# Kernel optimization log

Hardware: AMD Instinct MI355X
Metric: run time of the kernel (lower is better)

The kernel has to match this reference:

```python
import jax, jax.numpy as jnp
import numpy as np

LOG2 = float(np.log(2.0))
CUTOFF = 10.0
N, E, H, F, G = 50000, 800000, 64, 64, 50


def ssp(x):
    # ShiftedSoftplus
    return jax.nn.softplus(x) - LOG2


def setup_inputs() -> dict:
    key = jax.random.key(0)
    ks = jax.random.split(key, 20)
    s = 0.05
    inp = {
        'x0': jax.random.normal(ks[0], (N, H), jnp.float32),
        'x1': jax.random.normal(ks[1], (N, H), jnp.float32),
        'edge_index0': jax.random.randint(ks[2], (2, E), 0, N, jnp.int32),
        'edge_index1': jax.random.randint(ks[3], (2, E), 0, N, jnp.int32),
        'edge_weight0': jax.random.uniform(ks[4], (E,), jnp.float32) * CUTOFF,
        'edge_weight1': jax.random.uniform(ks[5], (E,), jnp.float32) * CUTOFF,
        'edge_attr0': jax.random.uniform(ks[6], (E, G), jnp.float32),
        'edge_attr1': jax.random.uniform(ks[7], (E, G), jnp.float32),
        # shared filter MLP (num_gaussians -> num_filters -> num_filters)
        'mlp_w1': jax.random.normal(ks[8], (G, F), jnp.float32) * s,
        'mlp_b1': jnp.zeros((F,), jnp.float32),
        'mlp_w2': jax.random.normal(ks[9], (F, F), jnp.float32) * s,
        'mlp_b2': jnp.zeros((F,), jnp.float32),
        # per-edge-type CFConv lin1 (H->F, no bias) and lin2 (F->H, bias)
        'lin1_w0': jax.random.normal(ks[10], (H, F), jnp.float32) * s,
        'lin2_w0': jax.random.normal(ks[11], (F, H), jnp.float32) * s,
        'lin2_b0': jnp.zeros((H,), jnp.float32),
        'lin1_w1': jax.random.normal(ks[12], (H, F), jnp.float32) * s,
        'lin2_w1': jax.random.normal(ks[13], (F, H), jnp.float32) * s,
        'lin2_b1': jnp.zeros((H,), jnp.float32),
        # trailing shared linear H->H
        'lin_w': jax.random.normal(ks[14], (H, H), jnp.float32) * s,
        'lin_b': jnp.zeros((H,), jnp.float32),
    }
    return inp


def cfconv(x, ei, ew, ea, l1w, l2w, l2b, mw1, mb1, mw2, mb2):
    # cosine cutoff on distances
    C = 0.5 * (jnp.cos(ew * (jnp.pi / CUTOFF)) + 1.0)  # [E]
    # filter MLP on RBF edge attrs: Linear -> SSP -> Linear
    W = (ssp(ea @ mw1 + mb1) @ mw2 + mb2) * C[:, None]  # [E,F]
    xs = x @ l1w                                        # [N,F]
    msg = xs[ei[0]] * W                                 # gather src, modulate
    agg = jax.ops.segment_sum(msg, ei[1], num_segments=x.shape[0])  # scatter-sum to dst
    return agg @ l2w + l2b                              # [N,H]


def reference(x0, x1, edge_index0, edge_index1, edge_weight0, edge_weight1,
              edge_attr0, edge_attr1, mlp_w1, mlp_b1, mlp_w2, mlp_b2,
              lin1_w0, lin2_w0, lin2_b0, lin1_w1, lin2_w1, lin2_b1,
              lin_w, lin_b):
    h0 = cfconv(x0, edge_index0, edge_weight0, edge_attr0,
                lin1_w0, lin2_w0, lin2_b0, mlp_w1, mlp_b1, mlp_w2, mlp_b2)
    h1 = cfconv(x1, edge_index1, edge_weight1, edge_attr1,
                lin1_w1, lin2_w1, lin2_b1, mlp_w1, mlp_b1, mlp_w2, mlp_b2)
    out0 = ssp(h0) @ lin_w + lin_b
    out1 = ssp(h1) @ lin_w + lin_b
    return out0, out1
```

## Files before the change

### kernel.cpp

```cpp
#include <hip/hip_runtime.h>
#include <math.h>

#define HD 64
#define GD 50
#define PAD 68

__device__ __forceinline__ float ssp_f(float x) {
    float ax = __builtin_fabsf(x);
    float e  = __expf(-ax);
    float sp = fmaxf(x, 0.0f) + __logf(1.0f + e);
    return sp - 0.69314718055994531f;
}

__global__ void __launch_bounds__(256) xs_kernel(const float* __restrict__ x,
                                                 const float* __restrict__ w,
                                                 float* __restrict__ xs,
                                                 float* __restrict__ agg, int N) {
    int wv = threadIdx.x >> 6;
    int j  = threadIdx.x & 63;
    int n  = blockIdx.x * 4 + wv;
    __shared__ float xr[4][64];
    if (n < N) xr[wv][j] = x[(size_t)n * HD + j];
    __syncthreads();
    if (n >= N) return;
    float acc = 0.0f;
#pragma unroll
    for (int k = 0; k < HD; ++k)
        acc = fmaf(xr[wv][k], w[k * HD + j], acc);
    xs[(size_t)n * HD + j] = acc;
    agg[(size_t)n * HD + j] = 0.0f;
}

#define EPW 64
#define WPB 2
__global__ void __launch_bounds__(WPB * 64, 2) edge_kernel(
        const float* __restrict__ ea, const float* __restrict__ ew,
        const int* __restrict__ ei, const float* __restrict__ xs,
        float* __restrict__ agg,
        const float* __restrict__ mw1, const float* __restrict__ mb1,
        const float* __restrict__ mw2, const float* __restrict__ mb2,
        int E) {
    const int wv   = threadIdx.x >> 6;
    const int lane = threadIdx.x & 63;
    const long ebase = ((long)blockIdx.x * WPB + wv) * EPW;

    __shared__ float wbuf[WPB][EPW * PAD];
    __shared__ int   sdst[WPB][EPW];
    __shared__ int   ssrc[WPB][EPW];

    long e = ebase + lane;
    bool valid = e < (long)E;
    long ec = valid ? e : (long)E - 1;

    const float2* ear2 = (const float2*)(ea + ec * GD);
    float h[HD];
#pragma unroll
    for (int f = 0; f < HD; ++f) h[f] = mb1[f];
    for (int gc = 0; gc < GD / 2; ++gc) {
        float2 v = ear2[gc];
        const float* wr = mw1 + 2 * gc * HD;
#pragma unroll
        for (int f = 0; f < HD; ++f) h[f] = fmaf(v.x, wr[f], h[f]);
#pragma unroll
        for (int f = 0; f < HD; ++f) h[f] = fmaf(v.y, wr[HD + f], h[f]);
    }

    float* hrow = &wbuf[wv][lane * PAD];
#pragma unroll
    for (int q = 0; q < HD / 4; ++q)
        *(float4*)(hrow + 4 * q) = make_float4(h[4*q], h[4*q+1], h[4*q+2], h[4*q+3]);

    float w[HD];
#pragma unroll
    for (int j = 0; j < HD; ++j) w[j] = mb2[j];
    for (int gb = 0; gb < HD / 4; ++gb) {
        float4 hv = *(const float4*)(hrow + 4 * gb);
        float s0 = ssp_f(hv.x), s1 = ssp_f(hv.y), s2 = ssp_f(hv.z), s3 = ssp_f(hv.w);
        const float* wr = mw2 + 4 * gb * HD;
#pragma unroll
        for (int j = 0; j < HD; ++j) w[j] = fmaf(s0, wr[j], w[j]);
#pragma unroll
        for (int j = 0; j < HD; ++j) w[j] = fmaf(s1, wr[HD + j], w[j]);
#pragma unroll
        for (int j = 0; j < HD; ++j) w[j] = fmaf(s2, wr[2 * HD + j], w[j]);
#pragma unroll
        for (int j = 0; j < HD; ++j) w[j] = fmaf(s3, wr[3 * HD + j], w[j]);
    }

    float cw = 0.5f * (__cosf(ew[ec] * 0.31415926535897931f) + 1.0f);
    if (!valid) cw = 0.0f;

#pragma unroll
    for (int q = 0; q < HD / 4; ++q)
        *(float4*)(hrow + 4 * q) = make_float4(w[4*q] * cw, w[4*q+1] * cw,
                                               w[4*q+2] * cw, w[4*q+3] * cw);
    sdst[wv][lane] = ei[(size_t)E + ec];
    ssrc[wv][lane] = ei[ec];
    __syncthreads();

#pragma unroll 8
    for (int t = 0; t < EPW; ++t) {
        int dst = sdst[wv][t];
        int src = ssrc[wv][t];
        float m = xs[(size_t)src * HD + lane] * wbuf[wv][t * PAD + lane];
        atomicAdd(&agg[(size_t)dst * HD + lane], m);
    }
}

__global__ void __launch_bounds__(256) out_kernel(
        const float* __restrict__ agg,
        const float* __restrict__ l2w, const float* __restrict__ l2b,
        const float* __restrict__ lw, const float* __restrict__ lb,
        float* __restrict__ out, int N) {
    int wv = threadIdx.x >> 6;
    int j  = threadIdx.x & 63;
    int n  = blockIdx.x * 4 + wv;
    __shared__ float buf[4][64];
    bool ok = n < N;
    if (ok) buf[wv][j] = agg[(size_t)n * HD + j];
    __syncthreads();
    float h = l2b[j];
#pragma unroll
    for (int g = 0; g < HD; ++g)
        h = fmaf(buf[wv][g], l2w[g * HD + j], h);
    h = ssp_f(h);
    __syncthreads();
    buf[wv][j] = h;
    __syncthreads();
    float o = lb[j];
#pragma unroll
    for (int g = 0; g < HD; ++g)
        o = fmaf(buf[wv][g], lw[g * HD + j], o);
    if (ok) out[(size_t)n * HD + j] = o;
}

extern "C" void kernel_launch(void* const* d_in, const int* in_sizes, int n_in,
                              void* d_out, int out_size, void* d_ws, size_t ws_size,
                              hipStream_t stream) {
    const float* x0   = (const float*)d_in[0];
    const float* x1   = (const float*)d_in[1];
    const int*   ei0  = (const int*)d_in[2];
    const int*   ei1  = (const int*)d_in[3];
    const float* ew0  = (const float*)d_in[4];
    const float* ew1  = (const float*)d_in[5];
    const float* ea0  = (const float*)d_in[6];
    const float* ea1  = (const float*)d_in[7];
    const float* mw1  = (const float*)d_in[8];
    const float* mb1  = (const float*)d_in[9];
    const float* mw2  = (const float*)d_in[10];
    const float* mb2  = (const float*)d_in[11];
    const float* l1w0 = (const float*)d_in[12];
    const float* l2w0 = (const float*)d_in[13];
    const float* l2b0 = (const float*)d_in[14];
    const float* l1w1 = (const float*)d_in[15];
    const float* l2w1 = (const float*)d_in[16];
    const float* l2b1 = (const float*)d_in[17];
    const float* lw   = (const float*)d_in[18];
    const float* lb   = (const float*)d_in[19];

    int N = in_sizes[0] / HD;
    int E = in_sizes[4];
    float* out = (float*)d_out;

    float* xs  = (float*)d_ws;
    float* agg = xs + (size_t)N * HD;

    int nodeBlocks = (N + 3) / 4;
    int edgeBlocks = (E + WPB * EPW - 1) / (WPB * EPW);

    for (int t = 0; t < 2; ++t) {
        const float* x   = t ? x1 : x0;
        const int*   ei  = t ? ei1 : ei0;
        const float* ew  = t ? ew1 : ew0;
        const float* ea  = t ? ea1 : ea0;
        const float* l1w = t ? l1w1 : l1w0;
        const float* l2w = t ? l2w1 : l2w0;
        const float* l2b = t ? l2b1 : l2b0;
        float* outp = out + (size_t)t * (size_t)N * HD;

        xs_kernel<<<nodeBlocks, 256, 0, stream>>>(x, l1w, xs, agg, N);
        edge_kernel<<<edgeBlocks, WPB * 64, 0, stream>>>(ea, ew, ei, xs, agg,
                                                         mw1, mb1, mw2, mb2, E);
        out_kernel<<<nodeBlocks, 256, 0, stream>>>(agg, l2w, l2b, lw, lb, outp, N);
    }
}
```

Baseline: 1.432 ms.

## Halve edge-kernel LDS staging buffer and raise occupancy target to four blocks

```diff
diff --git a/kernel.cpp b/kernel.cpp
--- a/kernel.cpp
+++ b/kernel.cpp
@@ -3,7 +3,7 @@
 
 #define HD 64
 #define GD 50
-#define PAD 68
+#define HALF 32
 
 __device__ __forceinline__ float ssp_f(float x) {
     float ax = __builtin_fabsf(x);
@@ -33,7 +33,7 @@
 
 #define EPW 64
 #define WPB 2
-__global__ void __launch_bounds__(WPB * 64, 2) edge_kernel(
+__global__ void __launch_bounds__(WPB * 64, 4) edge_kernel(
         const float* __restrict__ ea, const float* __restrict__ ew,
         const int* __restrict__ ei, const float* __restrict__ xs,
         float* __restrict__ agg,
@@ -44,7 +44,7 @@
     const int lane = threadIdx.x & 63;
     const long ebase = ((long)blockIdx.x * WPB + wv) * EPW;
 
-    __shared__ float wbuf[WPB][EPW * PAD];
+    __shared__ float wbuf[WPB][EPW * HALF];
     __shared__ int   sdst[WPB][EPW];
     __shared__ int   ssrc[WPB][EPW];
 
@@ -65,18 +65,37 @@
         for (int f = 0; f < HD; ++f) h[f] = fmaf(v.y, wr[HD + f], h[f]);
     }
 
-    float* hrow = &wbuf[wv][lane * PAD];
-#pragma unroll
-    for (int q = 0; q < HD / 4; ++q)
-        *(float4*)(hrow + 4 * q) = make_float4(h[4*q], h[4*q+1], h[4*q+2], h[4*q+3]);
+    float* hrow = &wbuf[wv][lane * HALF];
+#pragma unroll
+    for (int q = 0; q < HALF / 4; ++q)
+        *(float4*)(hrow + 4 * q) = make_float4(h[HALF + 4*q],     h[HALF + 4*q + 1],
+                                               h[HALF + 4*q + 2], h[HALF + 4*q + 3]);
 
     float w[HD];
 #pragma unroll
     for (int j = 0; j < HD; ++j) w[j] = mb2[j];
-    for (int gb = 0; gb < HD / 4; ++gb) {
+
+#pragma unroll
+    for (int gb = 0; gb < HALF / 4; ++gb) {
+        float s0 = ssp_f(h[4*gb + 0]);
+        float s1 = ssp_f(h[4*gb + 1]);
+        float s2 = ssp_f(h[4*gb + 2]);
+        float s3 = ssp_f(h[4*gb + 3]);
+        const float* wr = mw2 + 4 * gb * HD;
+#pragma unroll
+        for (int j = 0; j < HD; ++j) w[j] = fmaf(s0, wr[j], w[j]);
+#pragma unroll
+        for (int j = 0; j < HD; ++j) w[j] = fmaf(s1, wr[HD + j], w[j]);
+#pragma unroll
+        for (int j = 0; j < HD; ++j) w[j] = fmaf(s2, wr[2 * HD + j], w[j]);
+#pragma unroll
+        for (int j = 0; j < HD; ++j) w[j] = fmaf(s3, wr[3 * HD + j], w[j]);
+    }
+
+    for (int gb = 0; gb < HALF / 4; ++gb) {
         float4 hv = *(const float4*)(hrow + 4 * gb);
         float s0 = ssp_f(hv.x), s1 = ssp_f(hv.y), s2 = ssp_f(hv.z), s3 = ssp_f(hv.w);
-        const float* wr = mw2 + 4 * gb * HD;
+        const float* wr = mw2 + (HALF + 4 * gb) * HD;
 #pragma unroll
         for (int j = 0; j < HD; ++j) w[j] = fmaf(s0, wr[j], w[j]);
 #pragma unroll
@@ -90,20 +109,39 @@
     float cw = 0.5f * (__cosf(ew[ec] * 0.31415926535897931f) + 1.0f);
     if (!valid) cw = 0.0f;
 
-#pragma unroll
-    for (int q = 0; q < HD / 4; ++q)
-        *(float4*)(hrow + 4 * q) = make_float4(w[4*q] * cw, w[4*q+1] * cw,
-                                               w[4*q+2] * cw, w[4*q+3] * cw);
     sdst[wv][lane] = ei[(size_t)E + ec];
     ssrc[wv][lane] = ei[ec];
-    __syncthreads();
-
+
+    const int c  = lane & 31;
+    const int eh = lane & 32;
+
+#pragma unroll
+    for (int q = 0; q < HALF / 4; ++q)
+        *(float4*)(hrow + 4 * q) = make_float4(w[4*q] * cw,     w[4*q + 1] * cw,
+                                               w[4*q + 2] * cw, w[4*q + 3] * cw);
+    __syncthreads();
 #pragma unroll 8
-    for (int t = 0; t < EPW; ++t) {
-        int dst = sdst[wv][t];
-        int src = ssrc[wv][t];
-        float m = xs[(size_t)src * HD + lane] * wbuf[wv][t * PAD + lane];
-        atomicAdd(&agg[(size_t)dst * HD + lane], m);
+    for (int t = 0; t < EPW / 2; ++t) {
+        int idx = t + eh;
+        int dst = sdst[wv][idx];
+        int src = ssrc[wv][idx];
+        float m = xs[(size_t)src * HD + c] * wbuf[wv][idx * HALF + c];
+        atomicAdd(&agg[(size_t)dst * HD + c], m);
+    }
+    __syncthreads();
+
+#pragma unroll
+    for (int q = 0; q < HALF / 4; ++q)
+        *(float4*)(hrow + 4 * q) = make_float4(w[HALF + 4*q] * cw,     w[HALF + 4*q + 1] * cw,
+                                               w[HALF + 4*q + 2] * cw, w[HALF + 4*q + 3] * cw);
+    __syncthreads();
+#pragma unroll 8
+    for (int t = 0; t < EPW / 2; ++t) {
+        int idx = t + eh;
+        int dst = sdst[wv][idx];
+        int src = ssrc[wv][idx];
+        float m = xs[(size_t)src * HD + HALF + c] * wbuf[wv][idx * HALF + c];
+        atomicAdd(&agg[(size_t)dst * HD + HALF + c], m);
     }
 }
 
```

Result: faster. 1.362 ms (-4.9%).
